# Optimization experiments

Measured on AMD Instinct MI355X. Metric: run time of the kernel, lower is better.

## Reference

```python
import jax, jax.numpy as jnp
from jax import lax
import numpy as np

B, C, L, H, W = 2, 64, 16, 64, 64
K = 7
NG = 4  # GroupNorm groups (SpatialGroupNorm(4, channels))


def setup_inputs() -> dict:
    key = jax.random.key(0)
    ks = jax.random.split(key, 16)
    s = lambda i, shape, sc: jax.random.normal(ks[i], shape, jnp.float32) * sc
    return {
        "x": s(0, (B, C, L, H, W), 1.0),
        "dt": jax.random.uniform(ks[1], (B, L), jnp.float32, 0.1, 1.0),
        "W_sp": s(2, (C, C, K, K), 0.02),      # spatial 7x7 conv (OIHW)
        "W_dc": s(3, (C, C), 0.1),             # 1x1x1 depth conv
        "b_dc": jnp.zeros((C,), jnp.float32),
        "gn_g": jnp.ones((C,), jnp.float32),
        "gn_b": jnp.zeros((C,), jnp.float32),
        "W_in": s(4, (2 * C, C), 0.1),         # pw_conv_in 1x1 -> 2C (gated)
        "b_in": jnp.zeros((2 * C,), jnp.float32),
        "W_out": s(5, (C, C), 0.1),            # pw_conv_out 1x1
        "b_out": jnp.zeros((C,), jnp.float32),
        "nu_log": s(6, (C,), 0.5),             # LRU log decay rate
        "theta_log": s(7, (C,), 0.5),          # LRU log frequency
        "c_re": s(8, (C,), 0.5),               # LRU output mix (real)
        "c_im": s(9, (C,), 0.5),               # LRU output mix (imag)
        "d_skip": s(10, (C,), 0.5),            # LRU feedthrough
    }


def reference(x, dt, W_sp, W_dc, b_dc, gn_g, gn_b, W_in, b_in, W_out, b_out,
              nu_log, theta_log, c_re, c_im, d_skip):
    Bb, Cc, Ll, Hh, Ww = x.shape
    pad = W_sp.shape[-1] // 2
    # --- GatedConvBlock: FactorizedPeriodicConv3d (per-frame 2D conv) ---
    xf = x.transpose(0, 2, 1, 3, 4).reshape(Bb * Ll, Cc, Hh, Ww)  # [B*L,C,H,W]
    xp = jnp.pad(xf, ((0, 0), (0, 0), (0, 0), (pad, pad)), mode='wrap')    # circular W
    xp = jnp.pad(xp, ((0, 0), (0, 0), (pad, pad), (0, 0)), mode='edge')    # replicate H
    y = lax.conv_general_dilated(xp, W_sp, (1, 1), 'VALID',
                                 dimension_numbers=('NCHW', 'OIHW', 'NCHW'))
    y = jnp.einsum('nchw,oc->nohw', y, W_dc) + b_dc[None, :, None, None]   # depth 1x1x1
    # --- SpatialGroupNorm (per frame, 4 groups) ---
    g = y.reshape(Bb * Ll, NG, Cc // NG, Hh, Ww)
    mu = g.mean(axis=(2, 3, 4), keepdims=True)
    var = g.var(axis=(2, 3, 4), keepdims=True)
    y = ((g - mu) * lax.rsqrt(var + 1e-5)).reshape(Bb * Ll, Cc, Hh, Ww)
    y = y * gn_g[None, :, None, None] + gn_b[None, :, None, None]
    # --- gated pointwise convs + residual ---
    h = jnp.einsum('nchw,oc->nohw', y, W_in) + b_in[None, :, None, None]
    x1, x2 = jnp.split(h, 2, axis=1)
    z = x1 * jax.nn.sigmoid(x2)
    z = jnp.einsum('nchw,oc->nohw', z, W_out) + b_out[None, :, None, None]
    u = xf + z                                     # residual, [B*L,C,H,W]
    u = u.reshape(Bb, Ll, Cc, Hh, Ww).transpose(1, 0, 2, 3, 4)  # [L,B,C,H,W]
    # --- LRU: dt-dependent complex diagonal recurrence over L ---
    decay = jnp.exp(-jnp.exp(nu_log)[None, None, :] * dt[:, :, None])   # [B,L,C]
    phase = jnp.exp(theta_log)[None, None, :] * dt[:, :, None]          # [B,L,C]
    lam_re = (decay * jnp.cos(phase)).transpose(1, 0, 2)[..., None, None]  # [L,B,C,1,1]
    lam_im = (decay * jnp.sin(phase)).transpose(1, 0, 2)[..., None, None]
    gamma = jnp.sqrt(jnp.maximum(1.0 - decay ** 2, 1e-6)).transpose(1, 0, 2)[..., None, None]
    cr = c_re[None, :, None, None]
    ci = c_im[None, :, None, None]
    ds = d_skip[None, :, None, None]

    def step(carry, inputs):
        h_re, h_im = carry
        ut, lr, li, gm = inputs
        nr = lr * h_re - li * h_im + gm * ut
        ni = li * h_re + lr * h_im
        yt = cr * nr + ci * ni + ds * ut
        return (nr, ni), yt

    init = (jnp.zeros((Bb, Cc, Hh, Ww), x.dtype), jnp.zeros((Bb, Cc, Hh, Ww), x.dtype))
    _, ys = lax.scan(step, init, (u, lam_re, lam_im, gamma))   # ys: [L,B,C,H,W]
    return ys.transpose(1, 2, 0, 3, 4)                         # [B,C,L,H,W]
```

## Files before the change

kernel.cpp:

```cpp
#include <hip/hip_runtime.h>
#include <hip/hip_bf16.h>

typedef short bf16x8 __attribute__((ext_vector_type(8)));
typedef float f32x16 __attribute__((ext_vector_type(16)));

#define B_ 2
#define C_ 64
#define L_ 16
#define N_ 32
#define HW_ 4096

#define BY_WPH  0u
#define BY_WP1  401408u
#define BY_WP2  434176u
#define BY_OFF1 450560u
#define BY_LR   451072u
#define BY_LI   459264u
#define BY_GM   467456u
#define BY_PART 475648u
#define BY_XHI  524288u

__device__ __forceinline__ unsigned short f2bf(float v) {
    unsigned int u = __float_as_uint(v);
    unsigned int r = u + 0x7FFFu + ((u >> 16) & 1u);
    return (unsigned short)(r >> 16);
}
__device__ __forceinline__ float bf2f(unsigned short s) {
    return __uint_as_float(((unsigned int)s) << 16);
}

__global__ void k_setup(const float* __restrict__ W_sp, const float* __restrict__ W_dc,
                        unsigned short* __restrict__ WpH,
                        const float* __restrict__ W_in, const float* __restrict__ b_in,
                        const float* __restrict__ W_out,
                        const float* __restrict__ gn_g, const float* __restrict__ gn_b,
                        unsigned short* __restrict__ WP1, unsigned short* __restrict__ WP2,
                        float* __restrict__ OFF1,
                        const float* __restrict__ dt, const float* __restrict__ nu_log,
                        const float* __restrict__ theta_log,
                        float* __restrict__ lr_t, float* __restrict__ li_t,
                        float* __restrict__ gm_t) {
    int blk = blockIdx.x, tid = threadIdx.x;
    if (blk < 98) {
        int idx = blk * 256 + tid;
        if (idx >= 49 * 512) return;
        int lane = idx & 63;
        int ks   = (idx >> 6) & 3;
        int nf   = (idx >> 8) & 1;
        int tap  = idx >> 9;
        int oc   = nf * 32 + (lane & 31);
        int icb  = ks * 16 + (lane >> 5) * 8;
        unsigned short h8[8];
        #pragma unroll
        for (int e = 0; e < 8; ++e) {
            int ic = icb + e;
            float s = 0.f;
            for (int c = 0; c < 64; ++c)
                s += W_dc[oc * 64 + c] * W_sp[(c * 64 + ic) * 49 + tap];
            h8[e] = f2bf(s);
        }
        #pragma unroll
        for (int e = 0; e < 8; ++e) WpH[idx * 8 + e] = h8[e];
    } else if (blk < 111) {
        int idx = (blk - 98) * 256 + tid;
        if (idx < 2048) {
            int lane = idx & 63, ks = (idx >> 6) & 3, nf = (idx >> 8) & 3, hl = idx >> 10;
            int o = nf * 32 + (lane & 31), cb = ks * 16 + (lane >> 5) * 8;
            #pragma unroll
            for (int e = 0; e < 8; ++e) {
                float v = W_in[o * 64 + cb + e] * gn_g[cb + e];
                unsigned short h = f2bf(v);
                WP1[idx * 8 + e] = hl ? f2bf(v - bf2f(h)) : h;
            }
        } else if (idx < 3072) {
            int i2 = idx - 2048;
            int lane = i2 & 63, ks = (i2 >> 6) & 3, nf = (i2 >> 8) & 1, hl = i2 >> 9;
            int j = nf * 32 + (lane & 31), ob = ks * 16 + (lane >> 5) * 8;
            #pragma unroll
            for (int e = 0; e < 8; ++e) {
                float v = W_out[j * 64 + ob + e];
                unsigned short h = f2bf(v);
                WP2[i2 * 8 + e] = hl ? f2bf(v - bf2f(h)) : h;
            }
        } else if (idx < 3200) {
            int o = idx - 3072;
            float s = b_in[o];
            for (int c = 0; c < 64; ++c) s += W_in[o * 64 + c] * gn_b[c];
            OFF1[o] = s;
        }
    } else {
        int idx = (blk - 111) * 256 + tid;
        if (idx >= N_ * C_) return;
        int c = idx & 63, n = idx >> 6;
        float dtv = dt[n];
        float decay = expf(-expf(nu_log[c]) * dtv);
        float phase = expf(theta_log[c]) * dtv;
        lr_t[idx] = decay * cosf(phase);
        li_t[idx] = decay * sinf(phase);
        gm_t[idx] = sqrtf(fmaxf(1.f - decay * decay, 1e-6f));
    }
}

__global__ __launch_bounds__(256) void k_tr(const float* __restrict__ x,
                                            unsigned short* __restrict__ xhi) {
    __shared__ float t[64][129];
    int blk = blockIdx.x;
    int n = blk >> 5, seg = blk & 31;
    int p0 = seg * 128;
    int b = n >> 4, l = n & 15;
    int tid = threadIdx.x;
    for (int i = 0; i < 32; ++i) {
        int idx = i * 256 + tid;
        int ic = idx >> 7, p = idx & 127;
        t[ic][p] = x[(((size_t)(b * 64 + ic) * 16 + l)) * 4096 + p0 + p];
    }
    __syncthreads();
    for (int it = 0; it < 4; ++it) {
        int chunk = it * 256 + tid;
        int p = chunk >> 3, c0 = (chunk & 7) * 8;
        unsigned short h8[8];
        #pragma unroll
        for (int e = 0; e < 8; ++e) h8[e] = f2bf(t[c0 + e][p]);
        size_t off = ((size_t)(n * 4096 + p0 + p)) * 64 + c0;
        *(uint4*)&xhi[off] = *(uint4*)h8;
    }
}

__global__ __launch_bounds__(256, 2) void k_conv(
    const unsigned short* __restrict__ xhi,
    const unsigned short* __restrict__ WpH,
    const float* __restrict__ b_dc, unsigned short* __restrict__ y,
    float* __restrict__ part) {
    __shared__ uint4 halo[3904];
    __shared__ float ps[4][8], pq[4][8];
    int tid = threadIdx.x;
    int tile = blockIdx.x;
    int th = tile >> 2, tw = tile & 3;
    int n = blockIdx.y;
    int lane = tid & 63, wid = tid >> 6;
    int dh = (lane >> 4) & 1, dw = lane & 15, kslot = lane >> 5;

    for (int u2 = wid; u2 < 61; u2 += 4) {
        int row = u2 * 8 + (lane >> 3);
        if (row > 483) row = 483;
        int hh = row / 22, ww = row - hh * 22;
        int hs = th * 16 + hh - 3; hs = hs < 0 ? 0 : (hs > 63 ? 63 : hs);
        int wv = (tw * 16 + ww - 3) & 63;
        const uint4* src = (const uint4*)(xhi + ((size_t)n * 4096 + hs * 64 + wv) * 64) + (lane & 7);
        uint4 v = *src;
        *(uint4*)((char*)halo + ((row << 7) + (((lane & 7) ^ (row & 7)) << 4))) = v;
    }
    __syncthreads();

    f32x16 acc[2][2] = {};
    bf16x8 Aa[2][4], Ab[2][4], Ba[2][4], Bb[2][4];

#define LOADA(Areg, khv, kwv) { \
    _Pragma("unroll") for (int m = 0; m < 2; ++m) { \
        int rowb = (wid * 4 + 2 * m + dh + (khv)) * 22 + dw + (kwv); \
        _Pragma("unroll") for (int ks = 0; ks < 4; ++ks) { \
            int byt = (rowb << 7) + (((2 * ks + kslot) ^ (rowb & 7)) << 4); \
            Areg[m][ks] = *(const bf16x8*)((const char*)halo + byt); } } }

#define LOADB(Breg, tap) { \
    const bf16x8* WH = (const bf16x8*)WpH + (size_t)(tap) * 512 + lane; \
    _Pragma("unroll") for (int nf = 0; nf < 2; ++nf) \
        _Pragma("unroll") for (int ks = 0; ks < 4; ++ks) \
            Breg[nf][ks] = WH[(nf * 4 + ks) * 64]; }

#define MFMA_ALL(Areg, Breg) { \
    _Pragma("unroll") for (int ks = 0; ks < 4; ++ks) \
        _Pragma("unroll") for (int m = 0; m < 2; ++m) \
            _Pragma("unroll") for (int nf = 0; nf < 2; ++nf) \
                acc[m][nf] = __builtin_amdgcn_mfma_f32_32x32x16_bf16(Areg[m][ks], Breg[nf][ks], acc[m][nf], 0, 0, 0); }

    int kh = 0, kw = 0;
    LOADA(Aa, 0, 0); LOADB(Ba, 0);
    for (int t = 0; t < 48; t += 2) {
        ++kw; if (kw == 7) { kw = 0; ++kh; }
        LOADA(Ab, kh, kw);
        MFMA_ALL(Aa, Ba);
        LOADB(Bb, t + 1);
        ++kw; if (kw == 7) { kw = 0; ++kh; }
        LOADA(Aa, kh, kw);
        MFMA_ALL(Ab, Bb);
        LOADB(Ba, t + 2);
    }
    MFMA_ALL(Aa, Ba);
#undef LOADA
#undef LOADB
#undef MFMA_ALL

    int ocl = lane & 31;
    float sg[2], qg[2];
    #pragma unroll
    for (int nf = 0; nf < 2; ++nf) {
        float bv = b_dc[nf * 32 + ocl];
        float ss = 0.f, qq = 0.f;
        #pragma unroll
        for (int m = 0; m < 2; ++m) {
            #pragma unroll
            for (int j = 0; j < 16; ++j) {
                int r = (j & 3) + 8 * (j >> 2) + 4 * (lane >> 5);
                int h = th * 16 + wid * 4 + 2 * m + (r >> 4);
                int w = tw * 16 + (r & 15);
                float v = acc[m][nf][j] + bv;
                y[((size_t)n * 4096 + h * 64 + w) * 64 + nf * 32 + ocl] = f2bf(v);
                ss += v; qq += v * v;
            }
        }
        sg[nf] = ss; qg[nf] = qq;
    }
    #pragma unroll
    for (int off = 1; off < 16; off <<= 1) {
        sg[0] += __shfl_xor(sg[0], off);
        qg[0] += __shfl_xor(qg[0], off);
        sg[1] += __shfl_xor(sg[1], off);
        qg[1] += __shfl_xor(qg[1], off);
    }
    if ((lane & 15) == 0) {
        int cl = lane >> 4;
        int g0 = cl & 1, slot = wid * 2 + (cl >> 1);
        ps[g0][slot] = sg[0];     pq[g0][slot] = qg[0];
        ps[2 + g0][slot] = sg[1]; pq[2 + g0][slot] = qg[1];
    }
    __syncthreads();
    if (tid < 4) {
        float ss = 0.f, qq = 0.f;
        #pragma unroll
        for (int k2 = 0; k2 < 8; ++k2) { ss += ps[tid][k2]; qq += pq[tid][k2]; }
        part[((size_t)(n * 16 + tile)) * 8 + tid * 2]     = ss;
        part[((size_t)(n * 16 + tile)) * 8 + tid * 2 + 1] = qq;
    }
}

__global__ __launch_bounds__(256, 1) void k_pw(
    const unsigned short* __restrict__ y, const float* __restrict__ part,
    const unsigned short* __restrict__ WP1, const unsigned short* __restrict__ WP2,
    const float* __restrict__ OFF1, const float* __restrict__ b_out,
    unsigned short* __restrict__ xr ) {
    __shared__ __align__(16) char lds[4 * 8704];
    int tid = threadIdx.x, lane = tid & 63, wid = tid >> 6;
    int blk = blockIdx.x;
    int n = blk >> 5, sub = blk & 31;
    int ocl = lane & 31, hi5 = lane >> 5;
    int pixw = sub * 128 + wid * 32;
    char* myl = lds + wid * 8704;

    float mu[4], rsd[4];
    #pragma unroll
    for (int g = 0; g < 4; ++g) {
        float sm = 0.f, sq = 0.f;
        #pragma unroll
        for (int ch = 0; ch < 16; ++ch) {
            sm += part[(n * 16 + ch) * 8 + g * 2];
            sq += part[(n * 16 + ch) * 8 + g * 2 + 1];
        }
        float mean = sm * (1.f / 65536.f);
        float var  = sq * (1.f / 65536.f) - mean * mean;
        mu[g] = mean;
        rsd[g] = rsqrtf(var + 1e-5f);
    }

    const bf16x8* W1 = (const bf16x8*)WP1;
    const bf16x8* W2 = (const bf16x8*)WP2;

    int prow = pixw + ocl;

    bf16x8 A1[4];
    #pragma unroll
    for (int ks = 0; ks < 4; ++ks) {
        bf16x8 raw = *(const bf16x8*)&y[(size_t)(n * 4096 + prow) * 64 + ks * 16 + hi5 * 8];
        float m = mu[ks], r = rsd[ks];
        bf16x8 a;
        #pragma unroll
        for (int e = 0; e < 8; ++e)
            a[e] = (short)f2bf((bf2f((unsigned short)raw[e]) - m) * r);
        A1[ks] = a;
    }

    f32x16 acc1[4];
    #pragma unroll
    for (int nf = 0; nf < 4; ++nf) {
        float o0 = OFF1[nf * 32 + ocl];
        #pragma unroll
        for (int j = 0; j < 16; ++j) acc1[nf][j] = o0;
    }
    __builtin_amdgcn_s_setprio(1);
    #pragma unroll
    for (int ks = 0; ks < 4; ++ks)
        #pragma unroll
        for (int nf = 0; nf < 4; ++nf) {
            bf16x8 bh = W1[nf * 256 + ks * 64 + lane];
            bf16x8 bl = W1[1024 + nf * 256 + ks * 64 + lane];
            acc1[nf] = __builtin_amdgcn_mfma_f32_32x32x16_bf16(A1[ks], bh, acc1[nf], 0, 0, 0);
            acc1[nf] = __builtin_amdgcn_mfma_f32_32x32x16_bf16(A1[ks], bl, acc1[nf], 0, 0, 0);
        }
    __builtin_amdgcn_s_setprio(0);

    unsigned short* zp = (unsigned short*)myl;
    #pragma unroll
    for (int nf = 0; nf < 2; ++nf)
        #pragma unroll
        for (int j = 0; j < 16; ++j) {
            int r = (j & 3) + 8 * (j >> 2) + 4 * hi5;
            float x1 = acc1[nf][j], x2 = acc1[nf + 2][j];
            float z = x1 / (1.f + __expf(-x2));
            zp[r * 68 + nf * 32 + ocl] = f2bf(z);
        }
    asm volatile("s_waitcnt lgkmcnt(0)" ::: "memory");
    __builtin_amdgcn_sched_barrier(0);

    bf16x8 A2[4];
    #pragma unroll
    for (int ks = 0; ks < 4; ++ks)
        A2[ks] = *(const bf16x8*)(myl + ocl * 136 + ks * 32 + hi5 * 16);

    f32x16 acc2[2];
    #pragma unroll
    for (int nf = 0; nf < 2; ++nf)
        #pragma unroll
        for (int j = 0; j < 16; ++j) acc2[nf][j] = 0.f;
    __builtin_amdgcn_s_setprio(1);
    #pragma unroll
    for (int ks = 0; ks < 4; ++ks)
        #pragma unroll
        for (int nf = 0; nf < 2; ++nf) {
            bf16x8 bh = W2[nf * 256 + ks * 64 + lane];
            bf16x8 bl = W2[512 + nf * 256 + ks * 64 + lane];
            acc2[nf] = __builtin_amdgcn_mfma_f32_32x32x16_bf16(A2[ks], bh, acc2[nf], 0, 0, 0);
            acc2[nf] = __builtin_amdgcn_mfma_f32_32x32x16_bf16(A2[ks], bl, acc2[nf], 0, 0, 0);
        }
    __builtin_amdgcn_s_setprio(0);
    asm volatile("s_waitcnt lgkmcnt(0)" ::: "memory");
    __builtin_amdgcn_sched_barrier(0);

    float* up = (float*)myl;
    #pragma unroll
    for (int nf = 0; nf < 2; ++nf)
        #pragma unroll
        for (int j = 0; j < 16; ++j) {
            int r = (j & 3) + 8 * (j >> 2) + 4 * hi5;
            up[r * 68 + nf * 32 + ocl] = acc2[nf][j];
        }
    asm volatile("s_waitcnt lgkmcnt(0)" ::: "memory");
    __builtin_amdgcn_sched_barrier(0);

    {
        const float* rowp = up + ocl * 68 + hi5 * 32;
        float vrow[32];
        #pragma unroll
        for (int c4 = 0; c4 < 8; ++c4) {
            float4 v = *(const float4*)&rowp[c4 * 4];
            vrow[c4 * 4 + 0] = v.x; vrow[c4 * 4 + 1] = v.y;
            vrow[c4 * 4 + 2] = v.z; vrow[c4 * 4 + 3] = v.w;
        }
        int pixg = pixw + ocl;
        unsigned short* xrow = &xr[((size_t)(n * 4096 + pixg)) * 64 + hi5 * 32];
        bf16x8 xv0 = *(const bf16x8*)&xrow[0];
        bf16x8 xv1 = *(const bf16x8*)&xrow[8];
        bf16x8 xv2 = *(const bf16x8*)&xrow[16];
        bf16x8 xv3 = *(const bf16x8*)&xrow[24];
        unsigned short h16[32];
        #pragma unroll
        for (int e = 0; e < 8; ++e) {
            h16[e]      = f2bf(vrow[e]      + b_out[hi5 * 32 + e]      + bf2f((unsigned short)xv0[e]));
            h16[8 + e]  = f2bf(vrow[8 + e]  + b_out[hi5 * 32 + 8 + e]  + bf2f((unsigned short)xv1[e]));
            h16[16 + e] = f2bf(vrow[16 + e] + b_out[hi5 * 32 + 16 + e] + bf2f((unsigned short)xv2[e]));
            h16[24 + e] = f2bf(vrow[24 + e] + b_out[hi5 * 32 + 24 + e] + bf2f((unsigned short)xv3[e]));
        }
        *(uint4*)&xrow[0]  = *(uint4*)&h16[0];
        *(uint4*)&xrow[8]  = *(uint4*)&h16[8];
        *(uint4*)&xrow[16] = *(uint4*)&h16[16];
        *(uint4*)&xrow[24] = *(uint4*)&h16[24];
    }
    asm volatile("s_waitcnt lgkmcnt(0)" ::: "memory");
    __builtin_amdgcn_sched_barrier(0);
}

__global__ __launch_bounds__(256) void k_scan(
    const unsigned short* __restrict__ u16, const float* __restrict__ lr_t,
    const float* __restrict__ li_t, const float* __restrict__ gm_t,
    const float* __restrict__ c_re, const float* __restrict__ c_im,
    const float* __restrict__ d_skip, float* __restrict__ out) {
    __shared__ float us[2][16][36];
    int tid = threadIdx.x;
    int bid = blockIdx.x;
    int b = bid >> 9, h = (bid >> 3) & 63, wq = (bid >> 1) & 3, ch = bid & 1;
    int c2 = tid & 15, p = tid >> 4;
    int w = wq * 16 + p;
    int cbase = ch * 32 + c2 * 2;
    float2 cr2 = *(const float2*)&c_re[cbase];
    float2 ci2 = *(const float2*)&c_im[cbase];
    float2 ds2 = *(const float2*)&d_skip[cbase];
    float hr0 = 0.f, hi0 = 0.f, hr1 = 0.f, hi1 = 0.f;
    int wp = tid & 15, cc = tid >> 4;
    size_t ubase = ((size_t)(b * 16) * 4096 + h * 64 + w) * 64 + cbase;
    int lbase = (b * 16) * 64 + cbase;
    unsigned int uraw = *(const unsigned int*)&u16[ubase];
    float2 lr2 = *(const float2*)&lr_t[lbase];
    float2 li2 = *(const float2*)&li_t[lbase];
    float2 gm2 = *(const float2*)&gm_t[lbase];
    for (int l = 0; l < 16; ++l) {
        unsigned int urawn = 0;
        float2 lrn, lin, gmn;
        if (l < 15) {
            urawn = *(const unsigned int*)&u16[ubase + (size_t)(l + 1) * 262144];
            lrn = *(const float2*)&lr_t[lbase + (l + 1) * 64];
            lin = *(const float2*)&li_t[lbase + (l + 1) * 64];
            gmn = *(const float2*)&gm_t[lbase + (l + 1) * 64];
        }
        float ux = bf2f((unsigned short)(uraw & 0xffff));
        float uy = bf2f((unsigned short)(uraw >> 16));
        float nr0 = lr2.x * hr0 - li2.x * hi0 + gm2.x * ux;
        float ni0 = li2.x * hr0 + lr2.x * hi0;
        float y0  = cr2.x * nr0 + ci2.x * ni0 + ds2.x * ux; hr0 = nr0; hi0 = ni0;
        float nr1 = lr2.y * hr1 - li2.y * hi1 + gm2.y * uy;
        float ni1 = li2.y * hr1 + lr2.y * hi1;
        float y1  = cr2.y * nr1 + ci2.y * ni1 + ds2.y * uy; hr1 = nr1; hi1 = ni1;
        float2 st; st.x = y0; st.y = y1;
        *(float2*)&us[l & 1][p][c2 * 2] = st;
        __syncthreads();
        out[((size_t)(b * 64 + ch * 32 + cc * 2)     * 16 + l) * 4096 + h * 64 + wq * 16 + wp] = us[l & 1][wp][cc * 2];
        out[((size_t)(b * 64 + ch * 32 + cc * 2 + 1) * 16 + l) * 4096 + h * 64 + wq * 16 + wp] = us[l & 1][wp][cc * 2 + 1];
        uraw = urawn; lr2 = lrn; li2 = lin; gm2 = gmn;
    }
}

extern "C" void kernel_launch(void* const* d_in, const int* in_sizes, int n_in,
                              void* d_out, int out_size, void* d_ws, size_t ws_size,
                              hipStream_t stream) {
    const float* x        = (const float*)d_in[0];
    const float* dt       = (const float*)d_in[1];
    const float* W_sp     = (const float*)d_in[2];
    const float* W_dc     = (const float*)d_in[3];
    const float* b_dc     = (const float*)d_in[4];
    const float* gn_g     = (const float*)d_in[5];
    const float* gn_b     = (const float*)d_in[6];
    const float* W_in     = (const float*)d_in[7];
    const float* b_in     = (const float*)d_in[8];
    const float* W_out    = (const float*)d_in[9];
    const float* b_out    = (const float*)d_in[10];
    const float* nu_log   = (const float*)d_in[11];
    const float* theta_log= (const float*)d_in[12];
    const float* c_re     = (const float*)d_in[13];
    const float* c_im     = (const float*)d_in[14];
    const float* d_skip   = (const float*)d_in[15];

    char* ws = (char*)d_ws;
    unsigned short* WpH  = (unsigned short*)(ws + BY_WPH);
    unsigned short* WP1  = (unsigned short*)(ws + BY_WP1);
    unsigned short* WP2  = (unsigned short*)(ws + BY_WP2);
    float* OFF1   = (float*)(ws + BY_OFF1);
    float* lr_t   = (float*)(ws + BY_LR);
    float* li_t   = (float*)(ws + BY_LI);
    float* gm_t   = (float*)(ws + BY_GM);
    float* part   = (float*)(ws + BY_PART);
    unsigned short* xhi = (unsigned short*)(ws + BY_XHI);
    unsigned short* y16 = (unsigned short*)d_out;
    float* out    = (float*)d_out;

    hipLaunchKernelGGL(k_setup,   dim3(119),       dim3(256), 0, stream,
                       W_sp, W_dc, WpH, W_in, b_in, W_out, gn_g, gn_b, WP1, WP2, OFF1,
                       dt, nu_log, theta_log, lr_t, li_t, gm_t);
    hipLaunchKernelGGL(k_tr,      dim3(1024),      dim3(256), 0, stream, x, xhi);
    hipLaunchKernelGGL(k_conv,    dim3(16, 32),    dim3(256), 0, stream, xhi, WpH, b_dc, y16, part);
    hipLaunchKernelGGL(k_pw,      dim3(1024),      dim3(256), 0, stream, y16, part, WP1, WP2,
                       OFF1, b_out, xhi);
    hipLaunchKernelGGL(k_scan,    dim3(1024),      dim3(256), 0, stream, xhi, lr_t, li_t, gm_t,
                       c_re, c_im, d_skip, out);
}
```

Baseline: 126.8 us.

## Merge setup and transpose kernels, remap conv blocks, narrow scan per-thread channels

Folds the weight-setup kernel and the x transpose/bf16 conversion kernel into a single launch, which removes one launch and lets the small setup blocks run alongside the transpose blocks. The conv grid becomes 1D, with a block-index remap that interleaves frames across consecutive block IDs, apparently to spread work or improve cache locality across the device. The scan kernel moves from two channels per thread to one and doubles its grid, trading vectorized float2 loads for more parallelism and a smaller shared buffer. Giving the transpose a 33 KB shared array inside the merged kernel may also lower occupancy for the setup blocks.

```diff
diff --git a/kernel.cpp b/kernel.cpp
--- a/kernel.cpp
+++ b/kernel.cpp
@@ -29,21 +29,22 @@
     return __uint_as_float(((unsigned int)s) << 16);
 }
 
-__global__ void k_setup(const float* __restrict__ W_sp, const float* __restrict__ W_dc,
-                        unsigned short* __restrict__ WpH,
-                        const float* __restrict__ W_in, const float* __restrict__ b_in,
-                        const float* __restrict__ W_out,
-                        const float* __restrict__ gn_g, const float* __restrict__ gn_b,
-                        unsigned short* __restrict__ WP1, unsigned short* __restrict__ WP2,
-                        float* __restrict__ OFF1,
-                        const float* __restrict__ dt, const float* __restrict__ nu_log,
-                        const float* __restrict__ theta_log,
-                        float* __restrict__ lr_t, float* __restrict__ li_t,
-                        float* __restrict__ gm_t) {
+__global__ __launch_bounds__(256) void k_pre(
+    const float* __restrict__ W_sp, const float* __restrict__ W_dc,
+    unsigned short* __restrict__ WpH,
+    const float* __restrict__ W_in, const float* __restrict__ b_in,
+    const float* __restrict__ W_out,
+    const float* __restrict__ gn_g, const float* __restrict__ gn_b,
+    unsigned short* __restrict__ WP1, unsigned short* __restrict__ WP2,
+    float* __restrict__ OFF1,
+    const float* __restrict__ dt, const float* __restrict__ nu_log,
+    const float* __restrict__ theta_log,
+    float* __restrict__ lr_t, float* __restrict__ li_t, float* __restrict__ gm_t,
+    const float* __restrict__ x, unsigned short* __restrict__ xhi) {
+    __shared__ float t[64][129];
     int blk = blockIdx.x, tid = threadIdx.x;
     if (blk < 98) {
         int idx = blk * 256 + tid;
-        if (idx >= 49 * 512) return;
         int lane = idx & 63;
         int ks   = (idx >> 6) & 3;
         int nf   = (idx >> 8) & 1;
@@ -61,6 +62,7 @@
         }
         #pragma unroll
         for (int e = 0; e < 8; ++e) WpH[idx * 8 + e] = h8[e];
+        return;
     } else if (blk < 111) {
         int idx = (blk - 98) * 256 + tid;
         if (idx < 2048) {
@@ -88,7 +90,8 @@
             for (int c = 0; c < 64; ++c) s += W_in[o * 64 + c] * gn_b[c];
             OFF1[o] = s;
         }
-    } else {
+        return;
+    } else if (blk < 119) {
         int idx = (blk - 111) * 256 + tid;
         if (idx >= N_ * C_) return;
         int c = idx & 63, n = idx >> 6;
@@ -98,17 +101,12 @@
         lr_t[idx] = decay * cosf(phase);
         li_t[idx] = decay * sinf(phase);
         gm_t[idx] = sqrtf(fmaxf(1.f - decay * decay, 1e-6f));
-    }
-}
-
-__global__ __launch_bounds__(256) void k_tr(const float* __restrict__ x,
-                                            unsigned short* __restrict__ xhi) {
-    __shared__ float t[64][129];
-    int blk = blockIdx.x;
-    int n = blk >> 5, seg = blk & 31;
+        return;
+    }
+    int blk2 = blk - 119;
+    int n = blk2 >> 5, seg = blk2 & 31;
     int p0 = seg * 128;
     int b = n >> 4, l = n & 15;
-    int tid = threadIdx.x;
     for (int i = 0; i < 32; ++i) {
         int idx = i * 256 + tid;
         int ic = idx >> 7, p = idx & 127;
@@ -134,9 +132,11 @@
     __shared__ uint4 halo[3904];
     __shared__ float ps[4][8], pq[4][8];
     int tid = threadIdx.x;
-    int tile = blockIdx.x;
+    int lin = blockIdx.x;
+    int src = ((lin & 7) << 6) + (lin >> 3);
+    int n = src >> 4;
+    int tile = src & 15;
     int th = tile >> 2, tw = tile & 3;
-    int n = blockIdx.y;
     int lane = tid & 63, wid = tid >> 6;
     int dh = (lane >> 4) & 1, dw = lane & 15, kslot = lane >> 5;
 
@@ -146,8 +146,8 @@
         int hh = row / 22, ww = row - hh * 22;
         int hs = th * 16 + hh - 3; hs = hs < 0 ? 0 : (hs > 63 ? 63 : hs);
         int wv = (tw * 16 + ww - 3) & 63;
-        const uint4* src = (const uint4*)(xhi + ((size_t)n * 4096 + hs * 64 + wv) * 64) + (lane & 7);
-        uint4 v = *src;
+        const uint4* src4 = (const uint4*)(xhi + ((size_t)n * 4096 + hs * 64 + wv) * 64) + (lane & 7);
+        uint4 v = *src4;
         *(uint4*)((char*)halo + ((row << 7) + (((lane & 7) ^ (row & 7)) << 4))) = v;
     }
     __syncthreads();
@@ -238,7 +238,7 @@
     const unsigned short* __restrict__ y, const float* __restrict__ part,
     const unsigned short* __restrict__ WP1, const unsigned short* __restrict__ WP2,
     const float* __restrict__ OFF1, const float* __restrict__ b_out,
-    unsigned short* __restrict__ xr ) {
+    unsigned short* __restrict__ xr) {
     __shared__ __align__(16) char lds[4 * 8704];
     int tid = threadIdx.x, lane = tid & 63, wid = tid >> 6;
     int blk = blockIdx.x;
@@ -383,47 +383,36 @@
     const float* __restrict__ li_t, const float* __restrict__ gm_t,
     const float* __restrict__ c_re, const float* __restrict__ c_im,
     const float* __restrict__ d_skip, float* __restrict__ out) {
-    __shared__ float us[2][16][36];
+    __shared__ float us[2][16][17];
     int tid = threadIdx.x;
     int bid = blockIdx.x;
-    int b = bid >> 9, h = (bid >> 3) & 63, wq = (bid >> 1) & 3, ch = bid & 1;
-    int c2 = tid & 15, p = tid >> 4;
+    int b = bid >> 10, h = (bid >> 4) & 63, wq = (bid >> 2) & 3, ch = bid & 3;
+    int c16 = tid & 15, p = tid >> 4;
     int w = wq * 16 + p;
-    int cbase = ch * 32 + c2 * 2;
-    float2 cr2 = *(const float2*)&c_re[cbase];
-    float2 ci2 = *(const float2*)&c_im[cbase];
-    float2 ds2 = *(const float2*)&d_skip[cbase];
-    float hr0 = 0.f, hi0 = 0.f, hr1 = 0.f, hi1 = 0.f;
+    int cb = ch * 16 + c16;
+    float cr = c_re[cb], ci = c_im[cb], ds = d_skip[cb];
+    float hr = 0.f, hi = 0.f;
     int wp = tid & 15, cc = tid >> 4;
-    size_t ubase = ((size_t)(b * 16) * 4096 + h * 64 + w) * 64 + cbase;
-    int lbase = (b * 16) * 64 + cbase;
-    unsigned int uraw = *(const unsigned int*)&u16[ubase];
-    float2 lr2 = *(const float2*)&lr_t[lbase];
-    float2 li2 = *(const float2*)&li_t[lbase];
-    float2 gm2 = *(const float2*)&gm_t[lbase];
+    size_t ubase = ((size_t)(b * 16) * 4096 + h * 64 + w) * 64 + cb;
+    int lbase = (b * 16) * 64 + cb;
+    float uv = bf2f(u16[ubase]);
+    float lr = lr_t[lbase], li = li_t[lbase], gm = gm_t[lbase];
     for (int l = 0; l < 16; ++l) {
-        unsigned int urawn = 0;
-        float2 lrn, lin, gmn;
+        float uvn = 0.f, lrn = 0.f, lin2 = 0.f, gmn = 0.f;
         if (l < 15) {
-            urawn = *(const unsigned int*)&u16[ubase + (size_t)(l + 1) * 262144];
-            lrn = *(const float2*)&lr_t[lbase + (l + 1) * 64];
-            lin = *(const float2*)&li_t[lbase + (l + 1) * 64];
-            gmn = *(const float2*)&gm_t[lbase + (l + 1) * 64];
-        }
-        float ux = bf2f((unsigned short)(uraw & 0xffff));
-        float uy = bf2f((unsigned short)(uraw >> 16));
-        float nr0 = lr2.x * hr0 - li2.x * hi0 + gm2.x * ux;
-        float ni0 = li2.x * hr0 + lr2.x * hi0;
-        float y0  = cr2.x * nr0 + ci2.x * ni0 + ds2.x * ux; hr0 = nr0; hi0 = ni0;
-        float nr1 = lr2.y * hr1 - li2.y * hi1 + gm2.y * uy;
-        float ni1 = li2.y * hr1 + lr2.y * hi1;
-        float y1  = cr2.y * nr1 + ci2.y * ni1 + ds2.y * uy; hr1 = nr1; hi1 = ni1;
-        float2 st; st.x = y0; st.y = y1;
-        *(float2*)&us[l & 1][p][c2 * 2] = st;
+            uvn  = bf2f(u16[ubase + (size_t)(l + 1) * 262144]);
+            lrn  = lr_t[lbase + (l + 1) * 64];
+            lin2 = li_t[lbase + (l + 1) * 64];
+            gmn  = gm_t[lbase + (l + 1) * 64];
+        }
+        float nr = lr * hr - li * hi + gm * uv;
+        float ni = li * hr + lr * hi;
+        float yv = cr * nr + ci * ni + ds * uv;
+        hr = nr; hi = ni;
+        us[l & 1][p][c16] = yv;
         __syncthreads();
-        out[((size_t)(b * 64 + ch * 32 + cc * 2)     * 16 + l) * 4096 + h * 64 + wq * 16 + wp] = us[l & 1][wp][cc * 2];
-        out[((size_t)(b * 64 + ch * 32 + cc * 2 + 1) * 16 + l) * 4096 + h * 64 + wq * 16 + wp] = us[l & 1][wp][cc * 2 + 1];
-        uraw = urawn; lr2 = lrn; li2 = lin; gm2 = gmn;
+        out[((size_t)(b * 64 + ch * 16 + cc) * 16 + l) * 4096 + h * 64 + wq * 16 + wp] = us[l & 1][wp][cc];
+        uv = uvn; lr = lrn; li = lin2; gm = gmn;
     }
 }
 
@@ -460,13 +449,12 @@
     unsigned short* y16 = (unsigned short*)d_out;
     float* out    = (float*)d_out;
 
-    hipLaunchKernelGGL(k_setup,   dim3(119),       dim3(256), 0, stream,
+    hipLaunchKernelGGL(k_pre,     dim3(1143),      dim3(256), 0, stream,
                        W_sp, W_dc, WpH, W_in, b_in, W_out, gn_g, gn_b, WP1, WP2, OFF1,
-                       dt, nu_log, theta_log, lr_t, li_t, gm_t);
-    hipLaunchKernelGGL(k_tr,      dim3(1024),      dim3(256), 0, stream, x, xhi);
-    hipLaunchKernelGGL(k_conv,    dim3(16, 32),    dim3(256), 0, stream, xhi, WpH, b_dc, y16, part);
+                       dt, nu_log, theta_log, lr_t, li_t, gm_t, x, xhi);
+    hipLaunchKernelGGL(k_conv,    dim3(512),       dim3(256), 0, stream, xhi, WpH, b_dc, y16, part);
     hipLaunchKernelGGL(k_pw,      dim3(1024),      dim3(256), 0, stream, y16, part, WP1, WP2,
                        OFF1, b_out, xhi);
-    hipLaunchKernelGGL(k_scan,    dim3(1024),      dim3(256), 0, stream, xhi, lr_t, li_t, gm_t,
+    hipLaunchKernelGGL(k_scan,    dim3(2048),      dim3(256), 0, stream, xhi, lr_t, li_t, gm_t,
                        c_re, c_im, d_skip, out);
 }
```

Result: no change. 125.6 us (-0.9%).
